# Kernel optimization log

Hardware: AMD Instinct MI355X
Metric: run time of the kernel (lower is better)

Reference implementation:

```python
import jax, jax.numpy as jnp
import numpy as np

B, N, C = 8, 1024, 768
H = 12
DH = C // H  # 64
FF = 3072
EPS = 1e-5


def _layer_norm(x, gamma, beta):
    mu = jnp.mean(x, axis=-1, keepdims=True)
    var = jnp.mean(jnp.square(x - mu), axis=-1, keepdims=True)
    return (x - mu) * jax.lax.rsqrt(var + EPS) * gamma + beta


def setup_inputs() -> dict:
    key = jax.random.key(0)
    ks = jax.random.split(key, 16)
    s_in = 1.0 / np.sqrt(C)
    s_ff = 1.0 / np.sqrt(FF)
    return {
        "x": jax.random.normal(ks[0], (B, N, C), dtype=jnp.float32),
        "Wq": jax.random.uniform(ks[1], (C, C), jnp.float32, -s_in, s_in),
        "bq": jax.random.uniform(ks[2], (C,), jnp.float32, -s_in, s_in),
        "Wk": jax.random.uniform(ks[3], (C, C), jnp.float32, -s_in, s_in),
        "bk": jax.random.uniform(ks[4], (C,), jnp.float32, -s_in, s_in),
        "Wv": jax.random.uniform(ks[5], (C, C), jnp.float32, -s_in, s_in),
        "bv": jax.random.uniform(ks[6], (C,), jnp.float32, -s_in, s_in),
        "Wo": jax.random.uniform(ks[7], (C, C), jnp.float32, -s_in, s_in),
        "bo": jax.random.uniform(ks[8], (C,), jnp.float32, -s_in, s_in),
        "g1": jnp.ones((C,), jnp.float32),
        "b1": jnp.zeros((C,), jnp.float32),
        "g2": jnp.ones((C,), jnp.float32),
        "b2": jnp.zeros((C,), jnp.float32),
        "W1": jax.random.uniform(ks[9], (C, FF), jnp.float32, -s_in, s_in),
        "bf1": jax.random.uniform(ks[10], (FF,), jnp.float32, -s_in, s_in),
        "W2": jax.random.uniform(ks[11], (FF, C), jnp.float32, -s_ff, s_ff),
        "bf2": jax.random.uniform(ks[12], (C,), jnp.float32, -s_ff, s_ff),
    }


def reference(x, Wq, bq, Wk, bk, Wv, bv, Wo, bo, g1, b1, g2, b2, W1, bf1, W2, bf2):
    # Pre-norm attention block
    xn = _layer_norm(x, g1, b1)
    q = (xn @ Wq + bq).reshape(B, N, H, DH)
    k = (xn @ Wk + bk).reshape(B, N, H, DH)
    v = (xn @ Wv + bv).reshape(B, N, H, DH)
    scores = jnp.einsum("bqhd,bkhd->bhqk", q, k) / np.sqrt(DH)  # [B,H,N,N]
    attn = jax.nn.softmax(scores, axis=-1)
    z = jnp.einsum("bhqk,bkhd->bqhd", attn, v).reshape(B, N, C)
    attn_out = z @ Wo + bo
    b = x + attn_out  # dropout is identity (p=0 / eval)
    # Pre-norm MLP block
    bn = _layer_norm(b, g2, b2)
    h = jax.nn.relu(bn @ W1 + bf1)
    y = b + (h @ W2 + bf2)
    return y
```

## Files before the change

kernel.cpp:

```cpp
#include <hip/hip_runtime.h>
#include <hip/hip_bf16.h>

#define BDIM 8
#define SEQ  1024
#define CH   768
#define NHD  12
#define DHD  64
#define FFD  3072
#define MR   (BDIM*SEQ)

typedef __attribute__((ext_vector_type(8))) short bf16x8;
typedef __attribute__((ext_vector_type(4))) float f32x4;
typedef unsigned int   u32;
typedef unsigned short u16;

__device__ __forceinline__ u16 f2bfu(float x) {
  __hip_bfloat16 h = __float2bfloat16(x);
  return *reinterpret_cast<u16*>(&h);
}

__device__ __forceinline__ void glds16(const void* g, void* l) {
  __builtin_amdgcn_global_load_lds(
      (const __attribute__((address_space(1))) u32*)g,
      (__attribute__((address_space(3))) u32*)l, 16, 0, 0);
}

__global__ __launch_bounds__(256) void k_transpose_all(
    const float* __restrict__ Wq, const float* __restrict__ Wk,
    const float* __restrict__ Wv, const float* __restrict__ Wo,
    const float* __restrict__ W1, const float* __restrict__ W2,
    u16* __restrict__ ws) {
  __shared__ float tile[32][33];
  int b = blockIdx.x;
  int id, tb;
  if (b < 2304)      { id = b / 576; tb = b % 576; }
  else if (b < 4608) { id = 4;       tb = b - 2304; }
  else               { id = 5;       tb = b - 4608; }
  const float* src;
  u16* dst;
  int K, Nc;
  switch (id) {
    case 0: src = Wq; dst = ws;                      K = CH;  Nc = CH;  break;
    case 1: src = Wk; dst = ws + (size_t)CH*CH;      K = CH;  Nc = CH;  break;
    case 2: src = Wv; dst = ws + (size_t)2*CH*CH;    K = CH;  Nc = CH;  break;
    case 3: src = Wo; dst = ws + (size_t)3*CH*CH;    K = CH;  Nc = CH;  break;
    case 4: src = W1; dst = ws + (size_t)4*CH*CH;    K = CH;  Nc = FFD; break;
    default:src = W2; dst = ws + (size_t)4*CH*CH + (size_t)CH*FFD;
                                                     K = FFD; Nc = CH;  break;
  }
  int tilesx = Nc >> 5;
  int bx = (tb % tilesx) * 32;
  int by = (tb / tilesx) * 32;
  int tx = threadIdx.x & 31, ty = threadIdx.x >> 5;
#pragma unroll
  for (int j = 0; j < 32; j += 8)
    tile[ty + j][tx] = src[(size_t)(by + ty + j) * Nc + bx + tx];
  __syncthreads();
#pragma unroll
  for (int j = 0; j < 32; j += 8)
    dst[(size_t)(bx + ty + j) * K + by + tx] = f2bfu(tile[tx][ty + j]);
}

__global__ __launch_bounds__(256) void k_pack_bias(
    const float* __restrict__ bq, const float* __restrict__ bk,
    const float* __restrict__ bv, float* __restrict__ dst) {
  int i = blockIdx.x * 256 + threadIdx.x;
  if (i < 3 * CH)
    dst[i] = i < CH ? bq[i] : (i < 2 * CH ? bk[i - CH] : bv[i - 2 * CH]);
}

__global__ __launch_bounds__(256) void k_layernorm_bf16(
    const float* __restrict__ src, const float* __restrict__ gamma,
    const float* __restrict__ beta, u16* __restrict__ dst) {
  int row  = blockIdx.x * 4 + (threadIdx.x >> 6);
  int lane = threadIdx.x & 63;
  const float4* p4 = (const float4*)(src + (size_t)row * CH);
  float4 v[3];
  float s = 0.f, s2 = 0.f;
#pragma unroll
  for (int k = 0; k < 3; k++) {
    v[k] = p4[lane + k * 64];
    s  += v[k].x + v[k].y + v[k].z + v[k].w;
    s2 += v[k].x * v[k].x + v[k].y * v[k].y + v[k].z * v[k].z + v[k].w * v[k].w;
  }
#pragma unroll
  for (int m = 1; m < 64; m <<= 1) {
    s  += __shfl_xor(s,  m, 64);
    s2 += __shfl_xor(s2, m, 64);
  }
  float mean = s * (1.f / CH);
  float var  = s2 * (1.f / CH) - mean * mean;
  float rs   = rsqrtf(var + 1e-5f);
  u16* drow = dst + (size_t)row * CH;
#pragma unroll
  for (int k = 0; k < 3; k++) {
    int col = lane * 4 + k * 256;
    float4 gq = ((const float4*)gamma)[lane + k * 64];
    float4 bq = ((const float4*)beta )[lane + k * 64];
    u32 lo = (u32)f2bfu((v[k].x - mean) * rs * gq.x + bq.x) |
             ((u32)f2bfu((v[k].y - mean) * rs * gq.y + bq.y) << 16);
    u32 hi = (u32)f2bfu((v[k].z - mean) * rs * gq.z + bq.z) |
             ((u32)f2bfu((v[k].w - mean) * rs * gq.w + bq.w) << 16);
    uint2 w; w.x = lo; w.y = hi;
    *(uint2*)(drow + col) = w;
  }
}

#define GBN 128
#define GBK 32
enum { EPI_QKV = 0, EPI_RESID = 1, EPI_RELU = 2 };

template <int EPI, int TM = 128>
__global__ __launch_bounds__(256, 2) void k_gemm(
    const u16* __restrict__ A, const u16* __restrict__ Bt,
    const float* __restrict__ bias, const float* __restrict__ resid,
    void* __restrict__ outp, int K, int Nmat) {
  __shared__ u16 As[2][TM * GBK];
  __shared__ u16 Bs[2][GBN * GBK];
  constexpr int MF = TM / 32;
  int tid = threadIdx.x;
  int bm = blockIdx.x, bn = blockIdx.y;
  int lane = tid & 63, wid = tid >> 6;
  int wr = (wid >> 1) * (TM / 2), wc = (wid & 1) * 64;
  int lrow = lane & 15, g = lane >> 4;

  const u16* Abase = A + (size_t)(bm * TM) * K;
  const u16* Bbase = Bt + (size_t)(bn * GBN) * K;
  int srow = tid >> 2;
  int scol = (tid & 3) * 8;

  auto stage = [&](int buf, int k0) {
#pragma unroll
    for (int r = 0; r < TM / 64; r++)
      glds16(Abase + (size_t)(srow + r * 64) * K + k0 + scol,
             &As[buf][(tid + r * 256) * 8]);
#pragma unroll
    for (int r = 0; r < 2; r++)
      glds16(Bbase + (size_t)(srow + r * 64) * K + k0 + scol,
             &Bs[buf][(tid + r * 256) * 8]);
  };

  f32x4 acc[MF][4];
#pragma unroll
  for (int m = 0; m < MF; m++)
#pragma unroll
    for (int n = 0; n < 4; n++) acc[m][n] = {0.f, 0.f, 0.f, 0.f};

  int nk = K / GBK;
  stage(0, 0);
  for (int kt = 0; kt < nk; ++kt) {
    int buf = kt & 1;
    __syncthreads();
    if (kt + 1 < nk) stage(buf ^ 1, (kt + 1) * GBK);
    bf16x8 af[MF], bfr[4];
#pragma unroll
    for (int m = 0; m < MF; m++)
      af[m] = *(const bf16x8*)&As[buf][(wr + m * 16 + lrow) * GBK + g * 8];
#pragma unroll
    for (int n = 0; n < 4; n++)
      bfr[n] = *(const bf16x8*)&Bs[buf][(wc + n * 16 + lrow) * GBK + g * 8];
#pragma unroll
    for (int m = 0; m < MF; m++)
#pragma unroll
      for (int n = 0; n < 4; n++)
        acc[m][n] = __builtin_amdgcn_mfma_f32_16x16x32_bf16(af[m], bfr[n],
                                                            acc[m][n], 0, 0, 0);
  }

#pragma unroll
  for (int m = 0; m < MF; m++) {
    int row0 = bm * TM + wr + m * 16 + g * 4;
#pragma unroll
    for (int n = 0; n < 4; n++) {
      int col = bn * GBN + wc + n * 16 + lrow;
      float bval = bias[col];
      if constexpr (EPI == EPI_QKV) {
        int sel = col / CH;
        int c = col - sel * CH;
        int h = c >> 6, d = c & 63;
        int bb = row0 >> 10, nn0 = row0 & (SEQ - 1);
        if (sel == 2) {
          union { uint2 u; u16 h4[4]; } pk;
#pragma unroll
          for (int r = 0; r < 4; r++) pk.h4[r] = f2bfu(acc[m][n][r] + bval);
          *(uint2*)&((u16*)outp)[(size_t)2 * MR * CH +
                                 (((size_t)(bb * NHD + h)) * DHD + d) * SEQ +
                                 nn0] = pk.u;
        } else {
#pragma unroll
          for (int r = 0; r < 4; r++)
            ((u16*)outp)[(size_t)sel * MR * CH +
                         (((size_t)(bb * NHD + h)) * SEQ + nn0 + r) * DHD + d] =
                f2bfu(acc[m][n][r] + bval);
        }
      } else if constexpr (EPI == EPI_RESID) {
#pragma unroll
        for (int r = 0; r < 4; r++) {
          size_t idx = (size_t)(row0 + r) * Nmat + col;
          ((float*)outp)[idx] = acc[m][n][r] + bval + resid[idx];
        }
      } else {
#pragma unroll
        for (int r = 0; r < 4; r++) {
          float val = acc[m][n][r] + bval;
          ((u16*)outp)[(size_t)(row0 + r) * Nmat + col] =
              f2bfu(val > 0.f ? val : 0.f);
        }
      }
    }
  }
}

__global__ __launch_bounds__(256, 2) void k_attn(
    const u16* __restrict__ Q, const u16* __restrict__ Kk,
    const u16* __restrict__ Vt, u16* __restrict__ Z) {
  __shared__ u16 Ks[2][64 * 64];
  __shared__ u16 Vs[2][64 * 64];
  __shared__ u32 Psu[4][64 * 9];
  int tid = threadIdx.x, lane = tid & 63, wid = tid >> 6;
  int lrow = lane & 15, g = lane >> 4;
  int id  = blockIdx.y * 16 + blockIdx.x;
  int nid = (id & 7) * 192 + (id >> 3);
  int qtile = (nid & 15) * 64;
  int bh = nid >> 4;
  size_t base = (size_t)bh * SEQ * DHD;
  int bb = bh / NHD, hh = bh % NHD;
  int qrow0 = qtile + wid * 16;

  bf16x8 qf[2];
#pragma unroll
  for (int ks = 0; ks < 2; ks++)
    qf[ks] = *(const bf16x8*)(Q + base + (size_t)(qrow0 + lrow) * DHD +
                              ks * 32 + g * 8);

  f32x4 accO[4];
  float mrun = -1e30f, lrun = 0.f;
#pragma unroll
  for (int n = 0; n < 4; n++) accO[n] = {0.f, 0.f, 0.f, 0.f};

  int srow  = tid >> 3;
  int swz   = (((tid & 7) * 16) ^ ((srow & 7) << 4)) >> 1;
  const u16* kg0 = Kk + base + (size_t)srow * DHD + swz;
  const u16* vg0 = Vt + base + (size_t)srow * SEQ + swz;

  auto stageKV = [&](int buf, int t) {
    int kv0 = t * 64;
    const u16* kg = kg0 + (size_t)kv0 * DHD;
    glds16(kg,                    &Ks[buf][tid * 8]);
    glds16(kg + 32 * DHD,         &Ks[buf][2048 + tid * 8]);
    const u16* vg = vg0 + kv0;
    glds16(vg,                    &Vs[buf][tid * 8]);
    glds16(vg + 32 * SEQ,         &Vs[buf][2048 + tid * 8]);
  };

  int rc0 = ((g * 16)      ^ ((lrow & 7) << 4)) >> 1;
  int rc1 = ((64 + g * 16) ^ ((lrow & 7) << 4)) >> 1;

  stageKV(0, 0);
  for (int t = 0; t < 16; ++t) {
    int buf = t & 1;
    __syncthreads();
    if (t + 1 < 16) stageKV(buf ^ 1, t + 1);

    f32x4 sacc[4];
    __builtin_amdgcn_s_setprio(1);
#pragma unroll
    for (int n = 0; n < 4; n++) {
      bf16x8 kf0 = *(const bf16x8*)&Ks[buf][(n * 16 + lrow) * 64 + rc0];
      bf16x8 kf1 = *(const bf16x8*)&Ks[buf][(n * 16 + lrow) * 64 + rc1];
      sacc[n] = {0.f, 0.f, 0.f, 0.f};
      sacc[n] = __builtin_amdgcn_mfma_f32_16x16x32_bf16(kf0, qf[0], sacc[n], 0, 0, 0);
      sacc[n] = __builtin_amdgcn_mfma_f32_16x16x32_bf16(kf1, qf[1], sacc[n], 0, 0, 0);
    }
    __builtin_amdgcn_s_setprio(0);

    float mx = fmaxf(fmaxf(fmaxf(sacc[0][0], sacc[0][1]),
                           fmaxf(sacc[0][2], sacc[0][3])),
                     fmaxf(fmaxf(sacc[1][0], sacc[1][1]),
                           fmaxf(sacc[1][2], sacc[1][3])));
    mx = fmaxf(mx, fmaxf(fmaxf(fmaxf(sacc[2][0], sacc[2][1]),
                               fmaxf(sacc[2][2], sacc[2][3])),
                         fmaxf(fmaxf(sacc[3][0], sacc[3][1]),
                               fmaxf(sacc[3][2], sacc[3][3]))));
    mx *= 0.125f;
    mx = fmaxf(mx, __shfl_xor(mx, 16, 64));
    mx = fmaxf(mx, __shfl_xor(mx, 32, 64));

    if (__all(mx <= mrun + 8.f)) {
      float psum = 0.f;
#pragma unroll
      for (int n = 0; n < 4; n++)
#pragma unroll
        for (int r = 0; r < 4; r++) {
          float p = __expf(sacc[n][r] * 0.125f - mrun);
          sacc[n][r] = p;
          psum += p;
        }
      psum += __shfl_xor(psum, 16, 64);
      psum += __shfl_xor(psum, 32, 64);
      lrun += psum;
    } else {
      float mnew = fmaxf(mrun, mx);
      float alpha = __expf(mrun - mnew);
      float psum = 0.f;
#pragma unroll
      for (int n = 0; n < 4; n++)
#pragma unroll
        for (int r = 0; r < 4; r++) {
          float p = __expf(sacc[n][r] * 0.125f - mnew);
          sacc[n][r] = p;
          psum += p;
        }
      psum += __shfl_xor(psum, 16, 64);
      psum += __shfl_xor(psum, 32, 64);
      lrun = lrun * alpha + psum;
      mrun = mnew;
#pragma unroll
      for (int r = 0; r < 4; r++) {
        float ar = __shfl(alpha, (lane & 48) | (g * 4 + r), 64);
#pragma unroll
        for (int n = 0; n < 4; n++) accO[n][r] *= ar;
      }
    }

#pragma unroll
    for (int n = 0; n < 4; n++) {
      u32 lo = (u32)f2bfu(sacc[n][0]) | ((u32)f2bfu(sacc[n][1]) << 16);
      u32 hi = (u32)f2bfu(sacc[n][2]) | ((u32)f2bfu(sacc[n][3]) << 16);
      Psu[wid][lane * 9 + 2 * n]     = lo;
      Psu[wid][lane * 9 + 2 * n + 1] = hi;
    }

    int laneA = lrow + ((g & 1) << 5);
    int laneB = laneA + 16;
    int nsel = g >> 1;
    __builtin_amdgcn_s_setprio(1);
#pragma unroll
    for (int ks = 0; ks < 2; ks++) {
      int nks = 2 * ks + nsel;
      union { bf16x8 v; u32 w[4]; } pk;
      pk.w[0] = Psu[wid][laneA * 9 + 2 * nks];
      pk.w[1] = Psu[wid][laneA * 9 + 2 * nks + 1];
      pk.w[2] = Psu[wid][laneB * 9 + 2 * nks];
      pk.w[3] = Psu[wid][laneB * 9 + 2 * nks + 1];
      int rc = ks ? rc1 : rc0;
#pragma unroll
      for (int n = 0; n < 4; n++) {
        bf16x8 vf = *(const bf16x8*)&Vs[buf][(n * 16 + lrow) * 64 + rc];
        accO[n] = __builtin_amdgcn_mfma_f32_16x16x32_bf16(pk.v, vf,
                                                          accO[n], 0, 0, 0);
      }
    }
    __builtin_amdgcn_s_setprio(0);
  }

#pragma unroll
  for (int r = 0; r < 4; r++) {
    float lr = __shfl(lrun, (lane & 48) | (g * 4 + r), 64);
    float inv = 1.f / lr;
    int qrow = qrow0 + g * 4 + r;
#pragma unroll
    for (int n = 0; n < 4; n++) {
      int d = n * 16 + lrow;
      Z[((size_t)(bb * SEQ + qrow)) * CH + hh * DHD + d] =
          f2bfu(accO[n][r] * inv);
    }
  }
}

extern "C" void kernel_launch(void* const* d_in, const int* in_sizes, int n_in,
                              void* d_out, int out_size, void* d_ws,
                              size_t ws_size, hipStream_t stream) {
  (void)in_sizes; (void)n_in; (void)out_size; (void)ws_size;
  const float* x   = (const float*)d_in[0];
  const float* Wq  = (const float*)d_in[1];
  const float* bq  = (const float*)d_in[2];
  const float* Wk  = (const float*)d_in[3];
  const float* bk  = (const float*)d_in[4];
  const float* Wv  = (const float*)d_in[5];
  const float* bv  = (const float*)d_in[6];
  const float* Wo  = (const float*)d_in[7];
  const float* bo  = (const float*)d_in[8];
  const float* g1  = (const float*)d_in[9];
  const float* b1  = (const float*)d_in[10];
  const float* g2  = (const float*)d_in[11];
  const float* b2  = (const float*)d_in[12];
  const float* W1  = (const float*)d_in[13];
  const float* bf1 = (const float*)d_in[14];
  const float* W2  = (const float*)d_in[15];
  const float* bf2 = (const float*)d_in[16];

  u16* wsu  = (u16*)d_ws;
  u16* wq_t = wsu;
  u16* wo_t = wq_t + (size_t)3 * CH * CH;
  u16* w1_t = wo_t + (size_t)CH * CH;
  u16* w2_t = w1_t + (size_t)CH * FFD;
  u16* xn   = w2_t + (size_t)CH * FFD;
  u16* qb   = xn + (size_t)MR * CH;
  u16* zb   = qb + (size_t)3 * MR * CH;
  float* bres = (float*)(zb + (size_t)MR * CH);
  u16* hb   = qb;
  float* bqkv = (float*)d_out;

  dim3 blk(256);
  k_transpose_all<<<6912, blk, 0, stream>>>(Wq, Wk, Wv, Wo, W1, W2, wsu);
  k_pack_bias<<<9, blk, 0, stream>>>(bq, bk, bv, bqkv);

  k_layernorm_bf16<<<2048, blk, 0, stream>>>(x, g1, b1, xn);
  k_gemm<EPI_QKV><<<dim3(64, 18), blk, 0, stream>>>(xn, wq_t, bqkv, nullptr,
                                                    qb, CH, 3 * CH);
  k_attn<<<dim3(16, 96), blk, 0, stream>>>(qb, qb + (size_t)MR * CH,
                                           qb + (size_t)2 * MR * CH, zb);
  k_gemm<EPI_RESID, 64><<<dim3(128, 6), blk, 0, stream>>>(zb, wo_t, bo, x,
                                                          bres, CH, CH);
  k_layernorm_bf16<<<2048, blk, 0, stream>>>(bres, g2, b2, xn);
  k_gemm<EPI_RELU><<<dim3(64, 24), blk, 0, stream>>>(xn, w1_t, bf1, nullptr,
                                                     hb, CH, FFD);
  k_gemm<EPI_RESID, 64><<<dim3(128, 6), blk, 0, stream>>>(hb, w2_t, bf2, bres,
                                                          (float*)d_out, FFD, CH);
}
```

Baseline: 263.5 us.

## Replace GEMM with triple-buffered, swizzled-LDS kernel and workgroup reordering

The GEMM kernel becomes a 3-stage LDS ring. Loads are issued two k-tiles ahead and gated by explicit vmcnt waits, so one barrier per iteration replaces the double-buffer sync. LDS columns are XOR-swizzled to reduce bank conflicts, workgroup IDs are remapped for L2 locality, and MFMA priority is raised. The Wo and W2 projections drop from 64-row to 128-row tiles, halving their grid to 384 blocks. That may underfill the GPU, and the larger LDS footprint with occupancy hint 3 may raise register pressure.

```diff
diff --git a/kernel.cpp b/kernel.cpp
--- a/kernel.cpp
+++ b/kernel.cpp
@@ -106,73 +106,86 @@
   }
 }
 
-#define GBN 128
-#define GBK 32
 enum { EPI_QKV = 0, EPI_RESID = 1, EPI_RELU = 2 };
 
-template <int EPI, int TM = 128>
-__global__ __launch_bounds__(256, 2) void k_gemm(
+template <int EPI>
+__global__ __launch_bounds__(256, 3) void k_gemm3r(
     const u16* __restrict__ A, const u16* __restrict__ Bt,
     const float* __restrict__ bias, const float* __restrict__ resid,
     void* __restrict__ outp, int K, int Nmat) {
-  __shared__ u16 As[2][TM * GBK];
-  __shared__ u16 Bs[2][GBN * GBK];
-  constexpr int MF = TM / 32;
+  __shared__ u16 As[3][128 * 32];
+  __shared__ u16 Bs[3][128 * 32];
   int tid = threadIdx.x;
-  int bm = blockIdx.x, bn = blockIdx.y;
   int lane = tid & 63, wid = tid >> 6;
-  int wr = (wid >> 1) * (TM / 2), wc = (wid & 1) * 64;
+  int wm = wid >> 1, wn = wid & 1;
   int lrow = lane & 15, g = lane >> 4;
 
-  const u16* Abase = A + (size_t)(bm * TM) * K;
-  const u16* Bbase = Bt + (size_t)(bn * GBN) * K;
-  int srow = tid >> 2;
-  int scol = (tid & 3) * 8;
-
-  auto stage = [&](int buf, int k0) {
-#pragma unroll
-    for (int r = 0; r < TM / 64; r++)
-      glds16(Abase + (size_t)(srow + r * 64) * K + k0 + scol,
-             &As[buf][(tid + r * 256) * 8]);
-#pragma unroll
-    for (int r = 0; r < 2; r++)
-      glds16(Bbase + (size_t)(srow + r * 64) * K + k0 + scol,
-             &Bs[buf][(tid + r * 256) * 8]);
+  int nwg = gridDim.x * gridDim.y;
+  int id  = blockIdx.y * gridDim.x + blockIdx.x;
+  int swz = (id & 7) * (nwg >> 3) + (id >> 3);
+  int bm = swz % gridDim.x;
+  int bn = swz / gridDim.x;
+
+  const u16* Abase = A + (size_t)(bm * 128) * K;
+  const u16* Bbase = Bt + (size_t)(bn * 128) * K;
+
+  int r0 = tid >> 2;
+  int r1 = r0 + 64;
+  int s0 = (((tid & 3) ^ ((r0 >> 1) & 3)) * 8);
+  int s1 = (((tid & 3) ^ ((r1 >> 1) & 3)) * 8);
+
+  auto stage = [&](int slot, int kt) {
+    int k0 = kt * 32;
+    glds16(Abase + (size_t)r0 * K + k0 + s0, &As[slot][tid * 8]);
+    glds16(Abase + (size_t)r1 * K + k0 + s1, &As[slot][tid * 8 + 2048]);
+    glds16(Bbase + (size_t)r0 * K + k0 + s0, &Bs[slot][tid * 8]);
+    glds16(Bbase + (size_t)r1 * K + k0 + s1, &Bs[slot][tid * 8 + 2048]);
   };
 
-  f32x4 acc[MF][4];
-#pragma unroll
-  for (int m = 0; m < MF; m++)
+  int xsl  = (g ^ ((lrow >> 1) & 3)) * 8;
+  int arow = wm * 64 + lrow;
+  int brow = wn * 64 + lrow;
+
+  f32x4 acc[4][4];
+#pragma unroll
+  for (int m = 0; m < 4; m++)
 #pragma unroll
     for (int n = 0; n < 4; n++) acc[m][n] = {0.f, 0.f, 0.f, 0.f};
 
-  int nk = K / GBK;
+  int NK = K >> 5;
   stage(0, 0);
-  for (int kt = 0; kt < nk; ++kt) {
-    int buf = kt & 1;
-    __syncthreads();
-    if (kt + 1 < nk) stage(buf ^ 1, (kt + 1) * GBK);
-    bf16x8 af[MF], bfr[4];
-#pragma unroll
-    for (int m = 0; m < MF; m++)
-      af[m] = *(const bf16x8*)&As[buf][(wr + m * 16 + lrow) * GBK + g * 8];
-#pragma unroll
-    for (int n = 0; n < 4; n++)
-      bfr[n] = *(const bf16x8*)&Bs[buf][(wc + n * 16 + lrow) * GBK + g * 8];
-#pragma unroll
-    for (int m = 0; m < MF; m++)
-#pragma unroll
-      for (int n = 0; n < 4; n++)
-        acc[m][n] = __builtin_amdgcn_mfma_f32_16x16x32_bf16(af[m], bfr[n],
-                                                            acc[m][n], 0, 0, 0);
-  }
-
-#pragma unroll
-  for (int m = 0; m < MF; m++) {
-    int row0 = bm * TM + wr + m * 16 + g * 4;
-#pragma unroll
-    for (int n = 0; n < 4; n++) {
-      int col = bn * GBN + wc + n * 16 + lrow;
+  stage(1, 1);
+  for (int t = 0; t < NK; ++t) {
+    int slot = t % 3;
+    if (t < NK - 1) asm volatile("s_waitcnt vmcnt(4)" ::: "memory");
+    else            asm volatile("s_waitcnt vmcnt(0)" ::: "memory");
+    __builtin_amdgcn_s_barrier();
+    __builtin_amdgcn_sched_barrier(0);
+    if (t + 2 < NK) stage((t + 2) % 3, t + 2);
+
+    bf16x8 af[4], bfv[4];
+#pragma unroll
+    for (int mf = 0; mf < 4; mf++)
+      af[mf] = *(const bf16x8*)&As[slot][(arow + mf * 16) * 32 + xsl];
+#pragma unroll
+    for (int nf = 0; nf < 4; nf++)
+      bfv[nf] = *(const bf16x8*)&Bs[slot][(brow + nf * 16) * 32 + xsl];
+    __builtin_amdgcn_s_setprio(1);
+#pragma unroll
+    for (int mf = 0; mf < 4; mf++)
+#pragma unroll
+      for (int nf = 0; nf < 4; nf++)
+        acc[mf][nf] = __builtin_amdgcn_mfma_f32_16x16x32_bf16(
+            af[mf], bfv[nf], acc[mf][nf], 0, 0, 0);
+    __builtin_amdgcn_s_setprio(0);
+  }
+
+#pragma unroll
+  for (int mf = 0; mf < 4; mf++) {
+    int row0 = bm * 128 + wm * 64 + mf * 16 + g * 4;
+#pragma unroll
+    for (int nf = 0; nf < 4; nf++) {
+      int col = bn * 128 + wn * 64 + nf * 16 + lrow;
       float bval = bias[col];
       if constexpr (EPI == EPI_QKV) {
         int sel = col / CH;
@@ -182,7 +195,7 @@
         if (sel == 2) {
           union { uint2 u; u16 h4[4]; } pk;
 #pragma unroll
-          for (int r = 0; r < 4; r++) pk.h4[r] = f2bfu(acc[m][n][r] + bval);
+          for (int r = 0; r < 4; r++) pk.h4[r] = f2bfu(acc[mf][nf][r] + bval);
           *(uint2*)&((u16*)outp)[(size_t)2 * MR * CH +
                                  (((size_t)(bb * NHD + h)) * DHD + d) * SEQ +
                                  nn0] = pk.u;
@@ -191,18 +204,18 @@
           for (int r = 0; r < 4; r++)
             ((u16*)outp)[(size_t)sel * MR * CH +
                          (((size_t)(bb * NHD + h)) * SEQ + nn0 + r) * DHD + d] =
-                f2bfu(acc[m][n][r] + bval);
+                f2bfu(acc[mf][nf][r] + bval);
         }
       } else if constexpr (EPI == EPI_RESID) {
 #pragma unroll
         for (int r = 0; r < 4; r++) {
           size_t idx = (size_t)(row0 + r) * Nmat + col;
-          ((float*)outp)[idx] = acc[m][n][r] + bval + resid[idx];
+          ((float*)outp)[idx] = acc[mf][nf][r] + bval + resid[idx];
         }
       } else {
 #pragma unroll
         for (int r = 0; r < 4; r++) {
-          float val = acc[m][n][r] + bval;
+          float val = acc[mf][nf][r] + bval;
           ((u16*)outp)[(size_t)(row0 + r) * Nmat + col] =
               f2bfu(val > 0.f ? val : 0.f);
         }
@@ -246,11 +259,11 @@
   auto stageKV = [&](int buf, int t) {
     int kv0 = t * 64;
     const u16* kg = kg0 + (size_t)kv0 * DHD;
-    glds16(kg,                    &Ks[buf][tid * 8]);
-    glds16(kg + 32 * DHD,         &Ks[buf][2048 + tid * 8]);
+    glds16(kg,            &Ks[buf][tid * 8]);
+    glds16(kg + 32 * DHD, &Ks[buf][2048 + tid * 8]);
     const u16* vg = vg0 + kv0;
-    glds16(vg,                    &Vs[buf][tid * 8]);
-    glds16(vg + 32 * SEQ,         &Vs[buf][2048 + tid * 8]);
+    glds16(vg,            &Vs[buf][tid * 8]);
+    glds16(vg + 32 * SEQ, &Vs[buf][2048 + tid * 8]);
   };
 
   int rc0 = ((g * 16)      ^ ((lrow & 7) << 4)) >> 1;
@@ -407,15 +420,15 @@
   k_pack_bias<<<9, blk, 0, stream>>>(bq, bk, bv, bqkv);
 
   k_layernorm_bf16<<<2048, blk, 0, stream>>>(x, g1, b1, xn);
-  k_gemm<EPI_QKV><<<dim3(64, 18), blk, 0, stream>>>(xn, wq_t, bqkv, nullptr,
-                                                    qb, CH, 3 * CH);
+  k_gemm3r<EPI_QKV><<<dim3(64, 18), blk, 0, stream>>>(xn, wq_t, bqkv, nullptr,
+                                                      qb, CH, 3 * CH);
   k_attn<<<dim3(16, 96), blk, 0, stream>>>(qb, qb + (size_t)MR * CH,
                                            qb + (size_t)2 * MR * CH, zb);
-  k_gemm<EPI_RESID, 64><<<dim3(128, 6), blk, 0, stream>>>(zb, wo_t, bo, x,
-                                                          bres, CH, CH);
+  k_gemm3r<EPI_RESID><<<dim3(64, 6), blk, 0, stream>>>(zb, wo_t, bo, x, bres,
+                                                       CH, CH);
   k_layernorm_bf16<<<2048, blk, 0, stream>>>(bres, g2, b2, xn);
-  k_gemm<EPI_RELU><<<dim3(64, 24), blk, 0, stream>>>(xn, w1_t, bf1, nullptr,
-                                                     hb, CH, FFD);
-  k_gemm<EPI_RESID, 64><<<dim3(128, 6), blk, 0, stream>>>(hb, w2_t, bf2, bres,
-                                                          (float*)d_out, FFD, CH);
-}
+  k_gemm3r<EPI_RELU><<<dim3(64, 24), blk, 0, stream>>>(xn, w1_t, bf1, nullptr,
+                                                       hb, CH, FFD);
+  k_gemm3r<EPI_RESID><<<dim3(64, 6), blk, 0, stream>>>(hb, w2_t, bf2, bres,
+                                                       (float*)d_out, FFD, CH);
+}
```

After: 295.5 us. 1.12x slower.
